# Performance work log

Hardware: AMD Instinct MI355X
Metric: run time of the kernel (lower is better)

## Reference

```python
import jax, jax.numpy as jnp
import numpy as np

N = 100000        # nodes
E_HALF = 800000   # random edges before symmetrization
HID = 128         # hidden_dim
K = 4             # Chebyshev order
NEG = 0.01        # leaky_relu negative slope
BN_EPS = 1e-5
L2_EPS = 1e-12


def setup_inputs() -> dict:
    key = jax.random.key(0)
    ks = jax.random.split(key, 4)
    x = jax.random.normal(ks[0], (N, 3), dtype=jnp.float32)
    e = jax.random.randint(ks[1], (2, E_HALF), 0, N, dtype=jnp.int32)
    # symmetrize so the sym-normalized Laplacian is well defined
    edge_index = jnp.concatenate([e, e[::-1]], axis=1).astype(jnp.int64)

    def wcheb(k, fin, fout):
        return jax.random.normal(k, (K, fin, fout), dtype=jnp.float32) * np.float32(1.0 / np.sqrt(fin * K))

    wk = jax.random.split(ks[2], 5)
    return {
        "x": x, "edge_index": edge_index,
        "W1": wcheb(wk[0], 3, HID),   "b1": jnp.zeros((HID,), jnp.float32),
        "W2": wcheb(wk[1], HID, HID), "b2": jnp.zeros((HID,), jnp.float32),
        "W3": wcheb(wk[2], HID, HID), "b3": jnp.zeros((HID,), jnp.float32),
        "W4": wcheb(wk[3], HID, HID), "b4": jnp.zeros((HID,), jnp.float32),
        "g1": jnp.ones((HID,), jnp.float32), "be1": jnp.zeros((HID,), jnp.float32),
        "g2": jnp.ones((HID,), jnp.float32), "be2": jnp.zeros((HID,), jnp.float32),
        "g3": jnp.ones((HID,), jnp.float32), "be3": jnp.zeros((HID,), jnp.float32),
        "Wrep": jax.random.normal(wk[4], (HID, 3), dtype=jnp.float32) * np.float32(1.0 / np.sqrt(HID)),
        "brep": jnp.zeros((3,), jnp.float32),
    }


def _cheb(x, src, dst, norm, W, b):
    """PyG ChebConv (sym norm, lambda_max=2): out = sum_k T_k(L_hat) x @ W_k + b."""
    def prop(t):  # (L_hat t)_i = sum_{e: src->dst==i} norm_e * t[src_e]
        return jax.ops.segment_sum(t[src] * norm[:, None], dst, num_segments=N)
    Tx0 = x
    out = Tx0 @ W[0]
    Tx1 = prop(Tx0)
    out = out + Tx1 @ W[1]
    for k in range(2, W.shape[0]):
        Tx2 = 2.0 * prop(Tx1) - Tx0
        out = out + Tx2 @ W[k]
        Tx0, Tx1 = Tx1, Tx2
    return out + b


def _bn(x, g, b):  # BatchNorm1d, training mode (batch stats, biased var)
    mu = x.mean(axis=0)
    var = ((x - mu) ** 2).mean(axis=0)
    return (x - mu) * jax.lax.rsqrt(var + BN_EPS) * g + b


def _leaky(x):
    return jnp.where(x >= 0, x, NEG * x)


def reference(x, edge_index, W1, b1, W2, b2, W3, b3, W4, b4,
              g1, be1, g2, be2, g3, be3, Wrep, brep):
    src, dst = edge_index[0], edge_index[1]
    deg = jax.ops.segment_sum(jnp.ones(src.shape, jnp.float32), src, num_segments=N)
    dinv = jnp.where(deg > 0, jax.lax.rsqrt(jnp.maximum(deg, 1.0)), 0.0)
    # scaled Laplacian L_hat = -D^{-1/2} A D^{-1/2} (zero diagonal) for lambda_max=2
    norm = -(dinv[src] * dinv[dst])  # [E]

    h = _cheb(x.astype(jnp.float32), src, dst, norm, W1, b1)
    h = _bn(_leaky(h), g1, be1)
    h = _cheb(h, src, dst, norm, W2, b2)
    h = _bn(_leaky(h), g2, be2)
    h = _cheb(h, src, dst, norm, W3, b3)
    h = _bn(jnp.maximum(h, 0.0), g3, be3)
    h = _cheb(h, src, dst, norm, W4, b4)
    h = h / jnp.maximum(jnp.linalg.norm(h, axis=1, keepdims=True), L2_EPS)
    return h @ Wrep + brep  # [N, 3]
```

## Files before the change

kernel.cpp:

```cpp
#include <hip/hip_runtime.h>
#include <hip/hip_bf16.h>


#define HID 128
#define NEG 0.01f
#define BN_EPS 1e-5f
#define L2_EPS 1e-12f
#define CAP 64

typedef __attribute__((ext_vector_type(8))) short short8;
typedef __attribute__((ext_vector_type(4))) float floatx4;

__device__ __forceinline__ short f2bf(float f) {
    unsigned u = __float_as_uint(f);
    return (short)((u + 0x7fffu + ((u >> 16) & 1u)) >> 16);
}
__device__ __forceinline__ unsigned pack2bf(float x, float y) {
    return (unsigned)(unsigned short)f2bf(x) | ((unsigned)(unsigned short)f2bf(y) << 16);
}
__device__ __forceinline__ float bflo(unsigned u) { return __uint_as_float(u << 16); }
__device__ __forceinline__ float bfhi(unsigned u) { return __uint_as_float(u & 0xffff0000u); }
__device__ __forceinline__ float bf2f(unsigned short h) { return __uint_as_float((unsigned)h << 16); }

__device__ __forceinline__ float actf(float v, int act) {
    if (act == 0) return v >= 0.f ? v : NEG * v;
    if (act == 1) return v > 0.f ? v : 0.f;
    return v;
}


__global__ __launch_bounds__(256) void k_zero(int* __restrict__ deg0, float* __restrict__ S, int N) {
    int i = blockIdx.x * 256 + threadIdx.x;
    if (i < N) deg0[i] = 0;
    if (blockIdx.x == 0) {
        for (int k = threadIdx.x; k < 1024; k += 256) S[k] = 0.f;
    }
}

__global__ __launch_bounds__(256) void k_fillpad(const int* __restrict__ src, const int* __restrict__ dst,
                                                 int* __restrict__ slots, int* __restrict__ deg0, int E) {
    int e = blockIdx.x * 256 + threadIdx.x;
    if (e >= E) return;
    int d = dst[e];
    int s = src[e];
    int p = atomicAdd(&deg0[d], 1);
    if (p < CAP) slots[(size_t)d * CAP + p] = s;
}

__global__ __launch_bounds__(256) void k_dinv(const int* __restrict__ deg0, float* __restrict__ dinv,
                                              int* __restrict__ cnt, int N) {
    int i = blockIdx.x * 256 + threadIdx.x;
    if (i < N) {
        int d = deg0[i];
        dinv[i] = d > 0 ? rsqrtf((float)d) : 0.f;
        cnt[i] = d < CAP ? d : CAP;
    }
}

__global__ __launch_bounds__(256) void k_norm(const int* __restrict__ slots, const int* __restrict__ cnt,
                                              const float* __restrict__ dinv, int2* __restrict__ edges,
                                              float* __restrict__ snorm, int N) {
    int node = blockIdx.x * 4 + (threadIdx.x >> 6);
    if (node >= N) return;
    node = __builtin_amdgcn_readfirstlane(node);
    int lane = threadIdx.x & 63;
    int deg = cnt[node];
    float dd = dinv[node];
    int s = (lane < deg) ? slots[(size_t)node * CAP + lane] : 0;
    float w = (lane < deg) ? -(dinv[s] * dd) : 0.f;
    if (lane < deg) {
        int2 rec;
        rec.x = s;
        rec.y = __float_as_int(w);
        edges[(size_t)node * CAP + lane] = rec;
    }
    float sw = w;
    #pragma unroll
    for (int d = 1; d < 64; d <<= 1) sw += __shfl_xor(sw, d);
    if (lane == 0) snorm[node] = sw;
}

__global__ __launch_bounds__(256) void k_xpad(const float* __restrict__ x, float* __restrict__ xp, int N) {
    int i = blockIdx.x * 256 + threadIdx.x;
    if (i < N) {
        float4 v;
        v.x = x[(size_t)i * 3 + 0];
        v.y = x[(size_t)i * 3 + 1];
        v.z = x[(size_t)i * 3 + 2];
        v.w = 0.f;
        *(float4*)(xp + (size_t)i * 4) = v;
    }
}


__global__ __launch_bounds__(256) void k_prop3(const float* __restrict__ T, const float* __restrict__ prev,
                                               float* __restrict__ out, const int* __restrict__ cnt,
                                               const int2* __restrict__ edges,
                                               float a, float b, int N) {
    int i = blockIdx.x * 256 + threadIdx.x;
    if (i >= N) return;
    int deg = cnt[i];
    const int2* eb = edges + (size_t)i * CAP;
    float a0 = 0.f, a1 = 0.f, a2 = 0.f;
    int j = 0;
    for (; j + 4 <= deg; j += 4) {
        int2 r0 = eb[j + 0], r1 = eb[j + 1], r2 = eb[j + 2], r3 = eb[j + 3];
        float4 v0 = *(const float4*)(T + (size_t)r0.x * 4);
        float4 v1 = *(const float4*)(T + (size_t)r1.x * 4);
        float4 v2 = *(const float4*)(T + (size_t)r2.x * 4);
        float4 v3 = *(const float4*)(T + (size_t)r3.x * 4);
        float w0 = __int_as_float(r0.y), w1 = __int_as_float(r1.y);
        float w2 = __int_as_float(r2.y), w3 = __int_as_float(r3.y);
        a0 += w0 * v0.x + w1 * v1.x + w2 * v2.x + w3 * v3.x;
        a1 += w0 * v0.y + w1 * v1.y + w2 * v2.y + w3 * v3.y;
        a2 += w0 * v0.z + w1 * v1.z + w2 * v2.z + w3 * v3.z;
    }
    for (; j < deg; ++j) {
        int2 r = eb[j];
        float w = __int_as_float(r.y);
        float4 v = *(const float4*)(T + (size_t)r.x * 4);
        a0 += w * v.x;
        a1 += w * v.y;
        a2 += w * v.z;
    }
    float r0 = a * a0, r1 = a * a1, r2 = a * a2;
    if (prev) {
        const float* pp = prev + (size_t)i * 4;
        r0 += b * pp[0];
        r1 += b * pp[1];
        r2 += b * pp[2];
    }
    float4 o;
    o.x = r0; o.y = r1; o.z = r2; o.w = 0.f;
    *(float4*)(out + (size_t)i * 4) = o;
}

__global__ __launch_bounds__(256) void k_prop1(const unsigned* __restrict__ OUT,
                                               unsigned* __restrict__ T1, unsigned* __restrict__ T0,
                                               const int* __restrict__ cnt, const int2* __restrict__ edges,
                                               const float* __restrict__ snorm, const float* __restrict__ S,
                                               const float* __restrict__ g, const float* __restrict__ be,
                                               int act, float invN, int N) {
    int node = blockIdx.x * 4 + (threadIdx.x >> 6);
    if (node >= N) return;
    node = __builtin_amdgcn_readfirstlane(node);
    int lane = threadIdx.x & 63;
    int f0 = 2 * lane;
    float mu0 = S[f0] * invN, mu1 = S[f0 + 1] * invN;
    float v0 = S[f0 + 128] * invN - mu0 * mu0;
    float v1 = S[f0 + 129] * invN - mu1 * mu1;
    float a0 = g[f0] * rsqrtf(v0 + BN_EPS), a1 = g[f0 + 1] * rsqrtf(v1 + BN_EPS);
    float c0 = be[f0] - mu0 * a0, c1 = be[f0 + 1] - mu1 * a1;

    int deg = cnt[node];
    const int2* eb = edges + (size_t)node * CAP;
    float accx = 0.f, accy = 0.f;
    int j = 0;
    int nb = deg >> 3;
    if (nb > 0) {
        int2 recA[8]; unsigned tA[8];
        int2 recB[8]; unsigned tB[8];
        #pragma unroll
        for (int k = 0; k < 8; ++k) recA[k] = eb[k];
        #pragma unroll
        for (int k = 0; k < 8; ++k) tA[k] = OUT[(size_t)recA[k].x * 64 + lane];
        for (int bi = 1; bi < nb; ++bi) {
            const int2* ebb = eb + bi * 8;
            #pragma unroll
            for (int k = 0; k < 8; ++k) recB[k] = ebb[k];
            #pragma unroll
            for (int k = 0; k < 8; ++k) tB[k] = OUT[(size_t)recB[k].x * 64 + lane];
            #pragma unroll
            for (int k = 0; k < 8; ++k) {
                float w = __int_as_float(recA[k].y);
                accx += w * actf(bflo(tA[k]), act);
                accy += w * actf(bfhi(tA[k]), act);
            }
            #pragma unroll
            for (int k = 0; k < 8; ++k) { recA[k] = recB[k]; tA[k] = tB[k]; }
        }
        #pragma unroll
        for (int k = 0; k < 8; ++k) {
            float w = __int_as_float(recA[k].y);
            accx += w * actf(bflo(tA[k]), act);
            accy += w * actf(bfhi(tA[k]), act);
        }
        j = nb * 8;
    }
    for (; j < deg; ++j) {
        int2 r = eb[j];
        float w = __int_as_float(r.y);
        unsigned t0 = OUT[(size_t)r.x * 64 + lane];
        accx += w * actf(bflo(t0), act);
        accy += w * actf(bfhi(t0), act);
    }
    float si = snorm[node];
    __builtin_nontemporal_store(pack2bf(a0 * accx + si * c0, a1 * accy + si * c1),
                                &T1[(size_t)node * 64 + lane]);
    unsigned h = OUT[(size_t)node * 64 + lane];
    float t0lo = a0 * actf(bflo(h), act) + c0;
    float t0hi = a1 * actf(bfhi(h), act) + c1;
    __builtin_nontemporal_store(pack2bf(t0lo, t0hi), &T0[(size_t)node * 64 + lane]);
}

__global__ __launch_bounds__(256) void k_prop128(const unsigned* __restrict__ T, const unsigned* __restrict__ prev,
                                                 unsigned* __restrict__ out, const int* __restrict__ cnt,
                                                 const int2* __restrict__ edges,
                                                 float a, float b, int N) {
    int node = blockIdx.x * 4 + (threadIdx.x >> 6);
    if (node >= N) return;
    node = __builtin_amdgcn_readfirstlane(node);
    int lane = threadIdx.x & 63;
    int deg = cnt[node];
    const int2* eb = edges + (size_t)node * CAP;
    float accx = 0.f, accy = 0.f;
    int j = 0;
    int nb = deg >> 3;
    if (nb > 0) {
        int2 recA[8]; unsigned tA[8];
        int2 recB[8]; unsigned tB[8];
        #pragma unroll
        for (int k = 0; k < 8; ++k) recA[k] = eb[k];
        #pragma unroll
        for (int k = 0; k < 8; ++k) tA[k] = T[(size_t)recA[k].x * 64 + lane];
        for (int bi = 1; bi < nb; ++bi) {
            const int2* ebb = eb + bi * 8;
            #pragma unroll
            for (int k = 0; k < 8; ++k) recB[k] = ebb[k];
            #pragma unroll
            for (int k = 0; k < 8; ++k) tB[k] = T[(size_t)recB[k].x * 64 + lane];
            #pragma unroll
            for (int k = 0; k < 8; ++k) {
                float w = __int_as_float(recA[k].y);
                accx += w * bflo(tA[k]);
                accy += w * bfhi(tA[k]);
            }
            #pragma unroll
            for (int k = 0; k < 8; ++k) { recA[k] = recB[k]; tA[k] = tB[k]; }
        }
        #pragma unroll
        for (int k = 0; k < 8; ++k) {
            float w = __int_as_float(recA[k].y);
            accx += w * bflo(tA[k]);
            accy += w * bfhi(tA[k]);
        }
        j = nb * 8;
    }
    for (; j < deg; ++j) {
        int2 r = eb[j];
        float w = __int_as_float(r.y);
        unsigned t0 = T[(size_t)r.x * 64 + lane];
        accx += w * bflo(t0);
        accy += w * bfhi(t0);
    }
    float rx = a * accx, ry = a * accy;
    if (prev) {
        unsigned p = __builtin_nontemporal_load(&prev[(size_t)node * 64 + lane]);
        rx += b * bflo(p);
        ry += b * bfhi(p);
    }
    __builtin_nontemporal_store(pack2bf(rx, ry), &out[(size_t)node * 64 + lane]);
}


__global__ __launch_bounds__(256) void k_gemm1(const float* __restrict__ x, const float* __restrict__ t1,
                                               const float* __restrict__ t2, const float* __restrict__ t3,
                                               const float* __restrict__ W, const float* __restrict__ b,
                                               unsigned short* __restrict__ OUT, float* __restrict__ S,
                                               int npb, int N) {
    __shared__ float Wl[12 * 128];
    __shared__ float bl[128];
    __shared__ float sS[256];
    int tid = threadIdx.x;
    for (int i = tid; i < 1536; i += 256) Wl[i] = W[i];
    if (tid < 128) bl[tid] = b[tid];
    if (tid < 256) sS[tid] = 0.f;
    __syncthreads();
    int f = tid & 127;
    int base = blockIdx.x * npb;
    int end = base + npb < N ? base + npb : N;
    const float* rows[4] = {x, t1, t2, t3};
    float s1 = 0.f, s2 = 0.f;
    for (int node = base + (tid >> 7); node < end; node += 2) {
        float acc = bl[f];
        #pragma unroll
        for (int k = 0; k < 4; ++k) {
            float4 rv = *(const float4*)(rows[k] + (size_t)node * 4);
            acc += rv.x * Wl[(k * 3 + 0) * 128 + f];
            acc += rv.y * Wl[(k * 3 + 1) * 128 + f];
            acc += rv.z * Wl[(k * 3 + 2) * 128 + f];
        }
        unsigned short h = (unsigned short)f2bf(acc);
        OUT[(size_t)node * 128 + f] = h;
        float u = actf(bf2f(h), 0);
        s1 += u;
        s2 += u * u;
    }
    atomicAdd(&sS[f], s1);
    atomicAdd(&sS[f + 128], s2);
    __syncthreads();
    if (tid < 256) atomicAdd(&S[tid], sS[tid]);
}


__global__ __launch_bounds__(256) void k_packW(const float* __restrict__ WA, const float* __restrict__ WB,
                                               const float* __restrict__ WC, short* __restrict__ Wp) {
    int gid = blockIdx.x * 256 + threadIdx.x;
    int L = gid >> 16;
    int idx = gid & 65535;
    int j = idx & 7;
    int lane = (idx >> 3) & 63;
    int rest = idx >> 9;
    int nt = rest & 7;
    int ks = rest >> 3;
    int kk = ks * 32 + (lane >> 4) * 8 + j;
    int c = nt * 16 + (lane & 15);
    const float* W = (L == 0) ? WA : (L == 1) ? WB : WC;
    Wp[gid] = f2bf(W[(size_t)(kk >> 7) * 16384 + (kk & 127) * 128 + c]);
}

__global__ __launch_bounds__(512) void k_gemm512(const short* __restrict__ T0, const short* __restrict__ T1,
                                                 const short* __restrict__ T2, const short* __restrict__ T3,
                                                 const short* __restrict__ Wp, const float* __restrict__ bias,
                                                 unsigned short* __restrict__ OUT, float* __restrict__ S,
                                                 const float* __restrict__ Wrep, const float* __restrict__ brep,
                                                 float* __restrict__ fout,
                                                 int M, int doStats, int doFinal, int act) {
    __shared__ short Wlds[65536];
    __shared__ float sS[256];
    __shared__ float sW[388];
    int tid = threadIdx.x;
    int lane = tid & 63, wave = tid >> 6;
    if (tid < 256) sS[tid] = 0.f;
    if (doFinal) {
        for (int i = tid; i < 384; i += 512) sW[i] = Wrep[i];
        if (tid < 3) sW[384 + tid] = brep[tid];
    }
    for (int i = tid; i < 8192; i += 512) ((int4*)Wlds)[i] = ((const int4*)Wp)[i];
    __syncthreads();

    int quad = lane >> 4;
    int col0 = lane & 15;
    const short* Ts[4] = {T0, T1, T2, T3};
    float s1[8], s2[8];
    #pragma unroll
    for (int i = 0; i < 8; ++i) { s1[i] = 0.f; s2[i] = 0.f; }

    int nt32 = (M + 31) / 32;
    int stride = gridDim.x * 8;
    for (int t = blockIdx.x * 8 + wave; t < nt32; t += stride) {
        int r0 = t * 32;
        int rowa = r0 + col0;
        int rowb = rowa + 16;
        size_t rb0 = (size_t)(rowa < M ? rowa : M - 1) * 128;
        size_t rb1 = (size_t)(rowb < M ? rowb : M - 1) * 128;
        floatx4 acc0[8], acc1[8];
        #pragma unroll
        for (int i = 0; i < 8; ++i) {
            acc0[i][0] = 0.f; acc0[i][1] = 0.f; acc0[i][2] = 0.f; acc0[i][3] = 0.f;
            acc1[i][0] = 0.f; acc1[i][1] = 0.f; acc1[i][2] = 0.f; acc1[i][3] = 0.f;
        }
        #pragma unroll 4
        for (int ks = 0; ks < 16; ++ks) {
            const short* Tm = Ts[ks >> 2];
            int aoff = (ks & 3) * 32 + quad * 8;
            short8 af0 = *((const short8*)(Tm + rb0 + aoff));
            short8 af1 = *((const short8*)(Tm + rb1 + aoff));
            #pragma unroll
            for (int nt = 0; nt < 8; ++nt) {
                short8 bf = *((const short8*)(Wlds + ((ks * 8 + nt) * 64 + lane) * 8));
                acc0[nt] = __builtin_amdgcn_mfma_f32_16x16x32_bf16(af0, bf, acc0[nt], 0, 0, 0);
                acc1[nt] = __builtin_amdgcn_mfma_f32_16x16x32_bf16(af1, bf, acc1[nt], 0, 0, 0);
            }
        }
        if (doFinal) {
            #pragma unroll
            for (int half = 0; half < 2; ++half) {
                #pragma unroll
                for (int rg = 0; rg < 4; ++rg) {
                    int r = r0 + half * 16 + quad * 4 + rg;
                    float sq = 0.f, p0 = 0.f, p1 = 0.f, p2 = 0.f;
                    #pragma unroll
                    for (int nt = 0; nt < 8; ++nt) {
                        int c = nt * 16 + col0;
                        float v = (half ? acc1[nt][rg] : acc0[nt][rg]) + bias[c];
                        sq += v * v;
                        p0 += v * sW[c * 3 + 0];
                        p1 += v * sW[c * 3 + 1];
                        p2 += v * sW[c * 3 + 2];
                    }
                    #pragma unroll
                    for (int d = 1; d < 16; d <<= 1) {
                        sq += __shfl_xor(sq, d);
                        p0 += __shfl_xor(p0, d);
                        p1 += __shfl_xor(p1, d);
                        p2 += __shfl_xor(p2, d);
                    }
                    if (col0 == 0 && r < M) {
                        float inv = 1.f / fmaxf(sqrtf(sq), L2_EPS);
                        fout[r * 3 + 0] = p0 * inv + sW[384];
                        fout[r * 3 + 1] = p1 * inv + sW[385];
                        fout[r * 3 + 2] = p2 * inv + sW[386];
                    }
                }
            }
        } else {
            #pragma unroll
            for (int half = 0; half < 2; ++half) {
                int rbase = r0 + half * 16 + quad * 4;
                #pragma unroll
                for (int nt = 0; nt < 8; ++nt) {
                    int c = nt * 16 + col0;
                    float bv = bias[c];
                    #pragma unroll
                    for (int rg = 0; rg < 4; ++rg) {
                        int r = rbase + rg;
                        if (r < M) {
                            float v = (half ? acc1[nt][rg] : acc0[nt][rg]) + bv;
                            unsigned short h = (unsigned short)f2bf(v);
                            OUT[(size_t)r * 128 + c] = h;
                            float u = actf(bf2f(h), act);
                            s1[nt] += u;
                            s2[nt] += u * u;
                        }
                    }
                }
            }
        }
    }
    if (doStats) {
        #pragma unroll
        for (int nt = 0; nt < 8; ++nt) {
            int c = nt * 16 + col0;
            atomicAdd(&sS[c], s1[nt]);
            atomicAdd(&sS[c + 128], s2[nt]);
        }
        __syncthreads();
        if (tid < 256) atomicAdd(&S[tid], sS[tid]);
    }
}


extern "C" void kernel_launch(void* const* d_in, const int* in_sizes, int n_in,
                              void* d_out, int out_size, void* d_ws, size_t ws_size,
                              hipStream_t stream) {
    const int N = in_sizes[0] / 3;
    const int E = in_sizes[1] / 2;

    const float* x    = (const float*)d_in[0];
    const int*   ei   = (const int*)d_in[1];
    const int* esrc = ei;
    const int* edst = ei + E;
    const float* W1 = (const float*)d_in[2];  const float* b1 = (const float*)d_in[3];
    const float* W2 = (const float*)d_in[4];  const float* b2 = (const float*)d_in[5];
    const float* W3 = (const float*)d_in[6];  const float* b3 = (const float*)d_in[7];
    const float* W4 = (const float*)d_in[8];  const float* b4 = (const float*)d_in[9];
    const float* g1 = (const float*)d_in[10]; const float* be1 = (const float*)d_in[11];
    const float* g2 = (const float*)d_in[12]; const float* be2 = (const float*)d_in[13];
    const float* g3 = (const float*)d_in[14]; const float* be3 = (const float*)d_in[15];
    const float* Wrep = (const float*)d_in[16]; const float* brep = (const float*)d_in[17];
    float* out = (float*)d_out;

    char* w = (char*)d_ws;
    size_t off = 0;
    auto alloc = [&](size_t bytes) { size_t o = off; off = (off + bytes + 255) & ~(size_t)255; return o; };
    int*   arr    = (int*)(w + alloc((size_t)N * CAP * 4));
    int*   deg0   = (int*)(w + alloc((size_t)N * 4));
    int*   cnt    = (int*)(w + alloc((size_t)N * 4));
    float* dinv   = (float*)(w + alloc((size_t)N * 4));
    float* snorm  = (float*)(w + alloc((size_t)N * 4));
    int2*  edges  = (int2*)(w + alloc((size_t)N * CAP * 8));
    short* Wp     = (short*)(w + alloc(3 * 65536 * 2));
    float* S      = (float*)(w + alloc(4 * 256 * 4));
    float* xp     = (float*)(w + alloc((size_t)N * 4 * 4));
    float* t1f    = (float*)(w + alloc((size_t)N * 4 * 4));
    float* t2f    = (float*)(w + alloc((size_t)N * 4 * 4));
    float* t3f    = (float*)(w + alloc((size_t)N * 4 * 4));
    short* T0     = (short*)(w + alloc((size_t)N * 128 * 2));
    short* T1     = (short*)(w + alloc((size_t)N * 128 * 2));
    short* T2     = (short*)(w + alloc((size_t)N * 128 * 2));
    short* T3     = (short*)(w + alloc((size_t)N * 128 * 2));
    unsigned short* OUT = (unsigned short*)(w + alloc((size_t)N * 128 * 2));

    int gE = (E + 255) / 256;
    int gN = (N + 255) / 256;
    int gW = (N + 3) / 4;
    float invN = 1.f / (float)N;
    int npb = (N + 255) / 256;

    k_zero<<<gN, 256, 0, stream>>>(deg0, S, N);
    k_fillpad<<<gE, 256, 0, stream>>>(esrc, edst, arr, deg0, E);
    k_dinv<<<gN, 256, 0, stream>>>(deg0, dinv, cnt, N);
    k_norm<<<gW, 256, 0, stream>>>(arr, cnt, dinv, edges, snorm, N);
    k_packW<<<768, 256, 0, stream>>>(W2, W3, W4, Wp);
    k_xpad<<<gN, 256, 0, stream>>>(x, xp, N);

    k_prop3<<<gN, 256, 0, stream>>>(xp, nullptr, t1f, cnt, edges, 1.f, 0.f, N);
    k_prop3<<<gN, 256, 0, stream>>>(t1f, xp, t2f, cnt, edges, 2.f, -1.f, N);
    k_prop3<<<gN, 256, 0, stream>>>(t2f, t1f, t3f, cnt, edges, 2.f, -1.f, N);
    k_gemm1<<<256, 256, 0, stream>>>(xp, t1f, t2f, t3f, W1, b1, OUT, S, npb, N);

    const float* bs[3]  = {b2, b3, b4};
    const float* gs[3]  = {g2, g3, nullptr};
    const float* bes[3] = {be2, be3, nullptr};
    int actsIn[3] = {0, 0, 1};
    int actsOut[3] = {0, 1, 2};

    for (int l = 0; l < 3; ++l) {
        float* Sin = S + (size_t)l * 256;
        float* Sout = S + (size_t)(l + 1) * 256;
        const float* gc = (l == 0) ? g1 : gs[l - 1];
        const float* bc = (l == 0) ? be1 : bes[l - 1];
        k_prop1<<<gW, 256, 0, stream>>>((const unsigned*)OUT, (unsigned*)T1, (unsigned*)T0,
                                        cnt, edges, snorm, Sin, gc, bc, actsIn[l], invN, N);
        k_prop128<<<gW, 256, 0, stream>>>((const unsigned*)T1, (const unsigned*)T0, (unsigned*)T2,
                                          cnt, edges, 2.f, -1.f, N);
        k_prop128<<<gW, 256, 0, stream>>>((const unsigned*)T2, (const unsigned*)T1, (unsigned*)T3,
                                          cnt, edges, 2.f, -1.f, N);
        k_gemm512<<<256, 512, 0, stream>>>(T0, T1, T2, T3, Wp + (size_t)l * 65536, bs[l], OUT, Sout,
                                           Wrep, brep, out, N,
                                           l < 2 ? 1 : 0, l == 2 ? 1 : 0, actsOut[l]);
    }
}
```

Baseline: 1.090 ms.

## Partition edge bucketing by destination range and co-locate degree counter with slots

Edge bucketing now runs as NPART destination-range partitions. Each block scans a chunk of edges and only handles those whose destination falls in its partition, which keeps atomic and scatter traffic within a smaller memory window for better cache locality. The per-node degree counter moves into slot 0 of that node's padded adjacency row, so the atomic and the slot write hit the same cache line. In exchange, every edge's dst is read NPART times, and usable neighbour capacity drops from 64 to 63.

```diff
diff --git a/kernel.cpp b/kernel.cpp
--- a/kernel.cpp
+++ b/kernel.cpp
@@ -7,6 +7,8 @@
 #define BN_EPS 1e-5f
 #define L2_EPS 1e-12f
 #define CAP 64
+#define EPT 8
+#define NPART 8
 
 typedef __attribute__((ext_vector_type(8))) short short8;
 typedef __attribute__((ext_vector_type(4))) float floatx4;
@@ -29,35 +31,45 @@
 }
 
 
-__global__ __launch_bounds__(256) void k_zero(int* __restrict__ deg0, float* __restrict__ S, int N) {
+__global__ __launch_bounds__(256) void k_zero(int* __restrict__ arr, float* __restrict__ S, int N) {
     int i = blockIdx.x * 256 + threadIdx.x;
-    if (i < N) deg0[i] = 0;
+    if (i < N) arr[(size_t)i * CAP] = 0;
     if (blockIdx.x == 0) {
         for (int k = threadIdx.x; k < 1024; k += 256) S[k] = 0.f;
     }
 }
 
 __global__ __launch_bounds__(256) void k_fillpad(const int* __restrict__ src, const int* __restrict__ dst,
-                                                 int* __restrict__ slots, int* __restrict__ deg0, int E) {
-    int e = blockIdx.x * 256 + threadIdx.x;
-    if (e >= E) return;
-    int d = dst[e];
-    int s = src[e];
-    int p = atomicAdd(&deg0[d], 1);
-    if (p < CAP) slots[(size_t)d * CAP + p] = s;
-}
-
-__global__ __launch_bounds__(256) void k_dinv(const int* __restrict__ deg0, float* __restrict__ dinv,
+                                                 int* __restrict__ arr, int E, int part) {
+    int p = blockIdx.x & (NPART - 1);
+    int chunk = blockIdx.x >> 3;
+    int lo = p * part;
+    int hi = lo + part;
+    int base = chunk * (256 * EPT) + threadIdx.x;
+    #pragma unroll
+    for (int k = 0; k < EPT; ++k) {
+        int e = base + k * 256;
+        if (e < E) {
+            int d = dst[e];
+            if (d >= lo && d < hi) {
+                int pos = atomicAdd(&arr[(size_t)d * CAP], 1);
+                if (pos < CAP - 1) arr[(size_t)d * CAP + 1 + pos] = src[e];
+            }
+        }
+    }
+}
+
+__global__ __launch_bounds__(256) void k_dinv(const int* __restrict__ arr, float* __restrict__ dinv,
                                               int* __restrict__ cnt, int N) {
     int i = blockIdx.x * 256 + threadIdx.x;
     if (i < N) {
-        int d = deg0[i];
+        int d = arr[(size_t)i * CAP];
         dinv[i] = d > 0 ? rsqrtf((float)d) : 0.f;
-        cnt[i] = d < CAP ? d : CAP;
-    }
-}
-
-__global__ __launch_bounds__(256) void k_norm(const int* __restrict__ slots, const int* __restrict__ cnt,
+        cnt[i] = d < CAP - 1 ? d : CAP - 1;
+    }
+}
+
+__global__ __launch_bounds__(256) void k_norm(const int* __restrict__ arr, const int* __restrict__ cnt,
                                               const float* __restrict__ dinv, int2* __restrict__ edges,
                                               float* __restrict__ snorm, int N) {
     int node = blockIdx.x * 4 + (threadIdx.x >> 6);
@@ -66,7 +78,7 @@
     int lane = threadIdx.x & 63;
     int deg = cnt[node];
     float dd = dinv[node];
-    int s = (lane < deg) ? slots[(size_t)node * CAP + lane] : 0;
+    int s = (lane < deg) ? arr[(size_t)node * CAP + 1 + lane] : 0;
     float w = (lane < deg) ? -(dinv[s] * dd) : 0.f;
     if (lane < deg) {
         int2 rec;
@@ -465,7 +477,6 @@
     size_t off = 0;
     auto alloc = [&](size_t bytes) { size_t o = off; off = (off + bytes + 255) & ~(size_t)255; return o; };
     int*   arr    = (int*)(w + alloc((size_t)N * CAP * 4));
-    int*   deg0   = (int*)(w + alloc((size_t)N * 4));
     int*   cnt    = (int*)(w + alloc((size_t)N * 4));
     float* dinv   = (float*)(w + alloc((size_t)N * 4));
     float* snorm  = (float*)(w + alloc((size_t)N * 4));
@@ -482,15 +493,16 @@
     short* T3     = (short*)(w + alloc((size_t)N * 128 * 2));
     unsigned short* OUT = (unsigned short*)(w + alloc((size_t)N * 128 * 2));
 
-    int gE = (E + 255) / 256;
     int gN = (N + 255) / 256;
     int gW = (N + 3) / 4;
     float invN = 1.f / (float)N;
     int npb = (N + 255) / 256;
-
-    k_zero<<<gN, 256, 0, stream>>>(deg0, S, N);
-    k_fillpad<<<gE, 256, 0, stream>>>(esrc, edst, arr, deg0, E);
-    k_dinv<<<gN, 256, 0, stream>>>(deg0, dinv, cnt, N);
+    int part = (N + NPART - 1) / NPART;
+    int nchunk = (E + 256 * EPT - 1) / (256 * EPT);
+
+    k_zero<<<gN, 256, 0, stream>>>(arr, S, N);
+    k_fillpad<<<nchunk * NPART, 256, 0, stream>>>(esrc, edst, arr, E, part);
+    k_dinv<<<gN, 256, 0, stream>>>(arr, dinv, cnt, N);
     k_norm<<<gW, 256, 0, stream>>>(arr, cnt, dinv, edges, snorm, N);
     k_packW<<<768, 256, 0, stream>>>(W2, W3, W4, Wp);
     k_xpad<<<gN, 256, 0, stream>>>(x, xp, N);
```

After: 1.138 ms. 1.04x slower.
